# Performance work log

Measured on AMD Instinct MI355X. Metric: run time of the kernel, lower is better.

Reference implementation:

```python
import jax, jax.numpy as jnp
import numpy as np

NUM_HEADS = 8
DIM = 256  # == out_dim; module implicitly requires dim == out_dim


def setup_inputs() -> dict:
    key = jax.random.key(0)
    k0, k1, k2, k3, k4, k5 = jax.random.split(key, 6)
    B, N, T, dim = 4, 128, 128, DIM
    s = dim ** -0.5
    return {
        "v": jax.random.normal(k0, (B, N, T, dim), dtype=jnp.float32),
        "Wq": jax.random.normal(k1, (dim, dim), dtype=jnp.float32) * s,
        "Wk": jax.random.normal(k2, (dim, dim), dtype=jnp.float32) * s,
        "Wv": jax.random.normal(k3, (dim, dim), dtype=jnp.float32) * s,
        "Wp": jax.random.normal(k4, (dim, dim), dtype=jnp.float32) * s,
        "bp": jax.random.normal(k5, (dim,), dtype=jnp.float32) * 0.01,
    }


def reference(v, Wq, Wk, Wv, Wp, bp):
    B, N, T, dim = v.shape
    H = NUM_HEADS
    hd = dim // H
    scale = hd ** -0.5
    # projections (qkv_bias=False)
    q = (v @ Wq).reshape(B * N, T, H, hd)
    k = (v @ Wk).reshape(B * N, T, H, hd)
    vv = (v @ Wv).reshape(B * N, T, H, hd)
    # NOTE: heads axis is NOT moved before the matmul in the original torch
    # code, so attention is over the HEADS axis: per (b*n, t) an HxH matrix.
    attn = jnp.einsum('mthd,mtgd->mthg', q, k) * scale  # [B*N, T, H, H]
    attn = jax.nn.softmax(attn, axis=-1)
    x = jnp.einsum('mthg,mtgd->mthd', attn, vv).reshape(B, N, T, dim)
    # output projection (with bias); dropout probs are 0 / eval mode
    return x @ Wp + bp
```

## Files before the change

### kernel.cpp

```cpp
#include <hip/hip_runtime.h>
#include <hip/hip_bf16.h>
#include <math.h>


#define DIMX      256
#define NH        8
#define HD        32
#define TM        32
#define NTHREADS  256
#define ASTRIDE   264
#define QSTRIDE   776
#define NT_QKV    48
#define NT_P      16
#define KT        8

typedef __bf16 bf16x8 __attribute__((ext_vector_type(8)));
typedef __bf16 bf16x4 __attribute__((ext_vector_type(4)));
typedef float  f32x4  __attribute__((ext_vector_type(4)));

__global__ void pack_weights(const float* __restrict__ Wq,
                             const float* __restrict__ Wk,
                             const float* __restrict__ Wv,
                             const float* __restrict__ Wp,
                             __bf16* __restrict__ pk)
{
    const int QKV_FRAGS = NT_QKV * KT * 64;
    int u = blockIdx.x * blockDim.x + threadIdx.x;
    const float* W;
    int nt, kt, lane;
    if (u < QKV_FRAGS) {
        nt = u / (KT * 64); kt = (u / 64) % KT; lane = u % 64;
        if (nt < 16)      { W = Wq; }
        else if (nt < 32) { W = Wk; nt -= 16; }
        else              { W = Wv; nt -= 32; }
    } else {
        int u2 = u - QKV_FRAGS;
        nt = u2 / (KT * 64); kt = (u2 / 64) % KT; lane = u2 % 64;
        W = Wp;
    }
    const int n  = nt * 16 + (lane & 15);
    const int k0 = kt * 32 + (lane >> 4) * 8;
    bf16x8 frag;
#pragma unroll
    for (int j = 0; j < 8; ++j)
        frag[j] = (__bf16)W[(size_t)(k0 + j) * DIMX + n];
    *(bf16x8*)(pk + (size_t)u * 8) = frag;
}

__global__ __launch_bounds__(NTHREADS, 2)
void fused_attn_mfma(const float* __restrict__ v,
                     const __bf16* __restrict__ Wqkv_pk,
                     const __bf16* __restrict__ Wp_pk,
                     const float* __restrict__ bp,
                     float* __restrict__ out)
{
    __shared__ __align__(16) unsigned short smem[TM * ASTRIDE + TM * QSTRIDE];
    unsigned short* As  = smem;
    unsigned short* QKV = smem + TM * ASTRIDE;

    const int tid   = threadIdx.x;
    const int lane  = tid & 63;
    const int wv_id = tid >> 6;
    const int l15   = lane & 15;
    const int quad  = lane >> 4;
    const long token0 = (long)blockIdx.x * TM;

    {
        const float4* src = (const float4*)(v + token0 * DIMX);
#pragma unroll
        for (int i = 0; i < 8; ++i) {
            int u = tid + NTHREADS * i;
            int m = u >> 6;
            int c = (u & 63) * 4;
            float4 t4 = src[u];
            bf16x4 b4 = { (__bf16)t4.x, (__bf16)t4.y, (__bf16)t4.z, (__bf16)t4.w };
            *(bf16x4*)&As[m * ASTRIDE + c] = b4;
        }
    }
    __syncthreads();

    {
        const int nt0 = wv_id * 12;
        f32x4 acc[2][12];
#pragma unroll
        for (int tt = 0; tt < 2; ++tt)
#pragma unroll
            for (int j = 0; j < 12; ++j)
                acc[tt][j] = (f32x4){0.f, 0.f, 0.f, 0.f};

        for (int kt = 0; kt < KT; ++kt) {
            bf16x8 vf[2];
#pragma unroll
            for (int tt = 0; tt < 2; ++tt)
                vf[tt] = *(const bf16x8*)&As[(tt * 16 + l15) * ASTRIDE + kt * 32 + quad * 8];
            const bf16x8* wb = (const bf16x8*)Wqkv_pk + ((size_t)(nt0 * KT + kt) * 64 + lane);
#pragma unroll
            for (int j = 0; j < 12; ++j) {
                bf16x8 wf = wb[(size_t)j * KT * 64];
                acc[0][j] = __builtin_amdgcn_mfma_f32_16x16x32_bf16(wf, vf[0], acc[0][j], 0, 0, 0);
                acc[1][j] = __builtin_amdgcn_mfma_f32_16x16x32_bf16(wf, vf[1], acc[1][j], 0, 0, 0);
            }
        }
#pragma unroll
        for (int tt = 0; tt < 2; ++tt)
#pragma unroll
            for (int j = 0; j < 12; ++j) {
                bf16x4 p4 = { (__bf16)acc[tt][j][0], (__bf16)acc[tt][j][1],
                              (__bf16)acc[tt][j][2], (__bf16)acc[tt][j][3] };
                *(bf16x4*)&QKV[(tt * 16 + l15) * QSTRIDE + (nt0 + j) * 16 + quad * 4] = p4;
            }
    }
    __syncthreads();

    {
        const int ta = tid >> 3;
        const int h  = tid & 7;
        const float scale = 0.17677669529663687f;
        const unsigned short* qrow = &QKV[ta * QSTRIDE + h * HD];
        const unsigned short* kbase = &QKV[ta * QSTRIDE + 256];
        const unsigned short* vbase = &QKV[ta * QSTRIDE + 512];

        float q[HD];
#pragma unroll
        for (int s = 0; s < 4; ++s) {
            bf16x8 t = *(const bf16x8*)(qrow + s * 8);
#pragma unroll
            for (int j = 0; j < 8; ++j) q[s * 8 + j] = (float)t[j];
        }
        float logits[NH];
#pragma unroll
        for (int g = 0; g < NH; ++g) {
            float s = 0.f;
#pragma unroll
            for (int sg = 0; sg < 4; ++sg) {
                bf16x8 t = *(const bf16x8*)(kbase + g * HD + sg * 8);
#pragma unroll
                for (int j = 0; j < 8; ++j) s += q[sg * 8 + j] * (float)t[j];
            }
            logits[g] = s * scale;
        }
        float mx = logits[0];
#pragma unroll
        for (int g = 1; g < NH; ++g) mx = fmaxf(mx, logits[g]);
        float se = 0.f;
#pragma unroll
        for (int g = 0; g < NH; ++g) { logits[g] = __expf(logits[g] - mx); se += logits[g]; }
        float inv = 1.f / se;
#pragma unroll
        for (int g = 0; g < NH; ++g) logits[g] *= inv;

        float x[HD];
#pragma unroll
        for (int d = 0; d < HD; ++d) x[d] = 0.f;
#pragma unroll
        for (int g = 0; g < NH; ++g) {
            float p = logits[g];
#pragma unroll
            for (int sg = 0; sg < 4; ++sg) {
                bf16x8 t = *(const bf16x8*)(vbase + g * HD + sg * 8);
#pragma unroll
                for (int j = 0; j < 8; ++j) x[sg * 8 + j] += p * (float)t[j];
            }
        }
#pragma unroll
        for (int s = 0; s < 4; ++s) {
            bf16x8 o;
#pragma unroll
            for (int j = 0; j < 8; ++j) o[j] = (__bf16)x[s * 8 + j];
            *(bf16x8*)&As[ta * ASTRIDE + h * HD + s * 8] = o;
        }
    }
    __syncthreads();

    {
        const int nt0 = wv_id * 4;
        f32x4 acc[2][4];
#pragma unroll
        for (int tt = 0; tt < 2; ++tt)
#pragma unroll
            for (int j = 0; j < 4; ++j)
                acc[tt][j] = (f32x4){0.f, 0.f, 0.f, 0.f};

        for (int kt = 0; kt < KT; ++kt) {
            bf16x8 xf[2];
#pragma unroll
            for (int tt = 0; tt < 2; ++tt)
                xf[tt] = *(const bf16x8*)&As[(tt * 16 + l15) * ASTRIDE + kt * 32 + quad * 8];
            const bf16x8* wb = (const bf16x8*)Wp_pk + ((size_t)(nt0 * KT + kt) * 64 + lane);
#pragma unroll
            for (int j = 0; j < 4; ++j) {
                bf16x8 wf = wb[(size_t)j * KT * 64];
                acc[0][j] = __builtin_amdgcn_mfma_f32_16x16x32_bf16(wf, xf[0], acc[0][j], 0, 0, 0);
                acc[1][j] = __builtin_amdgcn_mfma_f32_16x16x32_bf16(wf, xf[1], acc[1][j], 0, 0, 0);
            }
        }
#pragma unroll
        for (int j = 0; j < 4; ++j) {
            f32x4 b = *(const f32x4*)&bp[(nt0 + j) * 16 + quad * 4];
#pragma unroll
            for (int tt = 0; tt < 2; ++tt) {
                f32x4 o = acc[tt][j] + b;
                *(f32x4*)&out[(token0 + tt * 16 + l15) * DIMX + (nt0 + j) * 16 + quad * 4] = o;
            }
        }
    }
}

extern "C" void kernel_launch(void* const* d_in, const int* in_sizes, int n_in,
                              void* d_out, int out_size, void* d_ws, size_t ws_size,
                              hipStream_t stream) {
    const float* v  = (const float*)d_in[0];
    const float* Wq = (const float*)d_in[1];
    const float* Wk = (const float*)d_in[2];
    const float* Wv = (const float*)d_in[3];
    const float* Wp = (const float*)d_in[4];
    const float* bp = (const float*)d_in[5];
    float* out = (float*)d_out;

    __bf16* pk = (__bf16*)d_ws;
    const __bf16* Wqkv_pk = pk;
    const __bf16* Wp_pk   = pk + (size_t)24576 * 8;

    pack_weights<<<128, 256, 0, stream>>>(Wq, Wk, Wv, Wp, pk);

    const int ntokens = in_sizes[0] / DIMX;
    fused_attn_mfma<<<ntokens / TM, NTHREADS, 0, stream>>>(v, Wqkv_pk, Wp_pk, bp, out);
}
```

Before: 188.1 us.

## Double block threads, split head attention across lane pairs, prefetch weight fragments

Raises the block to 512 threads, so each of 8 waves computes half as many MFMA output tiles in both projections. The per-head attention step is split across two lanes, each handling 16 of the 32 head dimensions, and the partial logits are combined with a shuffle. A software prefetch of the next k-step's weight fragments is added to hide global load latency. This lowers per-thread register pressure and lets more waves run concurrently, at the cost of an extra barrier and more redundant activation fragment loads per wave.

```diff
diff --git a/kernel.cpp b/kernel.cpp
--- a/kernel.cpp
+++ b/kernel.cpp
@@ -7,12 +7,13 @@
 #define NH        8
 #define HD        32
 #define TM        32
-#define NTHREADS  256
+#define NTHREADS  512
 #define ASTRIDE   264
 #define QSTRIDE   776
 #define NT_QKV    48
-#define NT_P      16
 #define KT        8
+#define NJ1       6
+#define NJ2       2
 
 typedef __bf16 bf16x8 __attribute__((ext_vector_type(8)));
 typedef __bf16 bf16x4 __attribute__((ext_vector_type(4)));
@@ -47,7 +48,7 @@
     *(bf16x8*)(pk + (size_t)u * 8) = frag;
 }
 
-__global__ __launch_bounds__(NTHREADS, 2)
+__global__ __launch_bounds__(NTHREADS, 4)
 void fused_attn_mfma(const float* __restrict__ v,
                      const __bf16* __restrict__ Wqkv_pk,
                      const __bf16* __restrict__ Wp_pk,
@@ -68,7 +69,7 @@
     {
         const float4* src = (const float4*)(v + token0 * DIMX);
 #pragma unroll
-        for (int i = 0; i < 8; ++i) {
+        for (int i = 0; i < 4; ++i) {
             int u = tid + NTHREADS * i;
             int m = u >> 6;
             int c = (u & 63) * 4;
@@ -80,31 +81,44 @@
     __syncthreads();
 
     {
-        const int nt0 = wv_id * 12;
-        f32x4 acc[2][12];
+        const int nt0 = wv_id * NJ1;
+        f32x4 acc[2][NJ1];
 #pragma unroll
         for (int tt = 0; tt < 2; ++tt)
 #pragma unroll
-            for (int j = 0; j < 12; ++j)
+            for (int j = 0; j < NJ1; ++j)
                 acc[tt][j] = (f32x4){0.f, 0.f, 0.f, 0.f};
 
+        const bf16x8* wb = (const bf16x8*)Wqkv_pk + lane;
+        bf16x8 wcur[NJ1];
+#pragma unroll
+        for (int j = 0; j < NJ1; ++j)
+            wcur[j] = wb[(size_t)((nt0 + j) * KT) * 64];
+
         for (int kt = 0; kt < KT; ++kt) {
+            const int ktn = (kt + 1 < KT) ? kt + 1 : KT - 1;
+            bf16x8 wnxt[NJ1];
+#pragma unroll
+            for (int j = 0; j < NJ1; ++j)
+                wnxt[j] = wb[(size_t)((nt0 + j) * KT + ktn) * 64];
+
             bf16x8 vf[2];
 #pragma unroll
             for (int tt = 0; tt < 2; ++tt)
                 vf[tt] = *(const bf16x8*)&As[(tt * 16 + l15) * ASTRIDE + kt * 32 + quad * 8];
-            const bf16x8* wb = (const bf16x8*)Wqkv_pk + ((size_t)(nt0 * KT + kt) * 64 + lane);
-#pragma unroll
-            for (int j = 0; j < 12; ++j) {
-                bf16x8 wf = wb[(size_t)j * KT * 64];
-                acc[0][j] = __builtin_amdgcn_mfma_f32_16x16x32_bf16(wf, vf[0], acc[0][j], 0, 0, 0);
-                acc[1][j] = __builtin_amdgcn_mfma_f32_16x16x32_bf16(wf, vf[1], acc[1][j], 0, 0, 0);
-            }
+
+#pragma unroll
+            for (int j = 0; j < NJ1; ++j) {
+                acc[0][j] = __builtin_amdgcn_mfma_f32_16x16x32_bf16(wcur[j], vf[0], acc[0][j], 0, 0, 0);
+                acc[1][j] = __builtin_amdgcn_mfma_f32_16x16x32_bf16(wcur[j], vf[1], acc[1][j], 0, 0, 0);
+            }
+#pragma unroll
+            for (int j = 0; j < NJ1; ++j) wcur[j] = wnxt[j];
         }
 #pragma unroll
         for (int tt = 0; tt < 2; ++tt)
 #pragma unroll
-            for (int j = 0; j < 12; ++j) {
+            for (int j = 0; j < NJ1; ++j) {
                 bf16x4 p4 = { (__bf16)acc[tt][j][0], (__bf16)acc[tt][j][1],
                               (__bf16)acc[tt][j][2], (__bf16)acc[tt][j][3] };
                 *(bf16x4*)&QKV[(tt * 16 + l15) * QSTRIDE + (nt0 + j) * 16 + quad * 4] = p4;
@@ -113,16 +127,19 @@
     __syncthreads();
 
     {
-        const int ta = tid >> 3;
-        const int h  = tid & 7;
+        const int ta  = tid >> 4;
+        const int sub = tid & 15;
+        const int h   = sub >> 1;
+        const int d0  = (sub & 1) * 16;
         const float scale = 0.17677669529663687f;
-        const unsigned short* qrow = &QKV[ta * QSTRIDE + h * HD];
-        const unsigned short* kbase = &QKV[ta * QSTRIDE + 256];
-        const unsigned short* vbase = &QKV[ta * QSTRIDE + 512];
-
-        float q[HD];
-#pragma unroll
-        for (int s = 0; s < 4; ++s) {
+
+        const unsigned short* qrow  = &QKV[ta * QSTRIDE + h * HD + d0];
+        const unsigned short* kbase = &QKV[ta * QSTRIDE + 256 + d0];
+        const unsigned short* vbase = &QKV[ta * QSTRIDE + 512 + d0];
+
+        float q[16];
+#pragma unroll
+        for (int s = 0; s < 2; ++s) {
             bf16x8 t = *(const bf16x8*)(qrow + s * 8);
 #pragma unroll
             for (int j = 0; j < 8; ++j) q[s * 8 + j] = (float)t[j];
@@ -132,13 +149,17 @@
         for (int g = 0; g < NH; ++g) {
             float s = 0.f;
 #pragma unroll
-            for (int sg = 0; sg < 4; ++sg) {
+            for (int sg = 0; sg < 2; ++sg) {
                 bf16x8 t = *(const bf16x8*)(kbase + g * HD + sg * 8);
 #pragma unroll
                 for (int j = 0; j < 8; ++j) s += q[sg * 8 + j] * (float)t[j];
             }
-            logits[g] = s * scale;
-        }
+            logits[g] = s;
+        }
+#pragma unroll
+        for (int g = 0; g < NH; ++g)
+            logits[g] = (logits[g] + __shfl_xor(logits[g], 1, 64)) * scale;
+
         float mx = logits[0];
 #pragma unroll
         for (int g = 1; g < NH; ++g) mx = fmaxf(mx, logits[g]);
@@ -149,53 +170,67 @@
 #pragma unroll
         for (int g = 0; g < NH; ++g) logits[g] *= inv;
 
-        float x[HD];
-#pragma unroll
-        for (int d = 0; d < HD; ++d) x[d] = 0.f;
+        float x[16];
+#pragma unroll
+        for (int d = 0; d < 16; ++d) x[d] = 0.f;
 #pragma unroll
         for (int g = 0; g < NH; ++g) {
             float p = logits[g];
 #pragma unroll
-            for (int sg = 0; sg < 4; ++sg) {
+            for (int sg = 0; sg < 2; ++sg) {
                 bf16x8 t = *(const bf16x8*)(vbase + g * HD + sg * 8);
 #pragma unroll
                 for (int j = 0; j < 8; ++j) x[sg * 8 + j] += p * (float)t[j];
             }
         }
-#pragma unroll
-        for (int s = 0; s < 4; ++s) {
+        __syncthreads();
+#pragma unroll
+        for (int s = 0; s < 2; ++s) {
             bf16x8 o;
 #pragma unroll
             for (int j = 0; j < 8; ++j) o[j] = (__bf16)x[s * 8 + j];
-            *(bf16x8*)&As[ta * ASTRIDE + h * HD + s * 8] = o;
+            *(bf16x8*)&As[ta * ASTRIDE + h * HD + d0 + s * 8] = o;
         }
     }
     __syncthreads();
 
     {
-        const int nt0 = wv_id * 4;
-        f32x4 acc[2][4];
+        const int nt0 = wv_id * NJ2;
+        f32x4 acc[2][NJ2];
 #pragma unroll
         for (int tt = 0; tt < 2; ++tt)
 #pragma unroll
-            for (int j = 0; j < 4; ++j)
+            for (int j = 0; j < NJ2; ++j)
                 acc[tt][j] = (f32x4){0.f, 0.f, 0.f, 0.f};
 
+        const bf16x8* wb = (const bf16x8*)Wp_pk + lane;
+        bf16x8 wcur[NJ2];
+#pragma unroll
+        for (int j = 0; j < NJ2; ++j)
+            wcur[j] = wb[(size_t)((nt0 + j) * KT) * 64];
+
         for (int kt = 0; kt < KT; ++kt) {
+            const int ktn = (kt + 1 < KT) ? kt + 1 : KT - 1;
+            bf16x8 wnxt[NJ2];
+#pragma unroll
+            for (int j = 0; j < NJ2; ++j)
+                wnxt[j] = wb[(size_t)((nt0 + j) * KT + ktn) * 64];
+
             bf16x8 xf[2];
 #pragma unroll
             for (int tt = 0; tt < 2; ++tt)
                 xf[tt] = *(const bf16x8*)&As[(tt * 16 + l15) * ASTRIDE + kt * 32 + quad * 8];
-            const bf16x8* wb = (const bf16x8*)Wp_pk + ((size_t)(nt0 * KT + kt) * 64 + lane);
-#pragma unroll
-            for (int j = 0; j < 4; ++j) {
-                bf16x8 wf = wb[(size_t)j * KT * 64];
-                acc[0][j] = __builtin_amdgcn_mfma_f32_16x16x32_bf16(wf, xf[0], acc[0][j], 0, 0, 0);
-                acc[1][j] = __builtin_amdgcn_mfma_f32_16x16x32_bf16(wf, xf[1], acc[1][j], 0, 0, 0);
-            }
-        }
-#pragma unroll
-        for (int j = 0; j < 4; ++j) {
+
+#pragma unroll
+            for (int j = 0; j < NJ2; ++j) {
+                acc[0][j] = __builtin_amdgcn_mfma_f32_16x16x32_bf16(wcur[j], xf[0], acc[0][j], 0, 0, 0);
+                acc[1][j] = __builtin_amdgcn_mfma_f32_16x16x32_bf16(wcur[j], xf[1], acc[1][j], 0, 0, 0);
+            }
+#pragma unroll
+            for (int j = 0; j < NJ2; ++j) wcur[j] = wnxt[j];
+        }
+#pragma unroll
+        for (int j = 0; j < NJ2; ++j) {
             f32x4 b = *(const f32x4*)&bp[(nt0 + j) * 16 + quad * 4];
 #pragma unroll
             for (int tt = 0; tt < 2; ++tt) {
@@ -221,7 +256,7 @@
     const __bf16* Wqkv_pk = pk;
     const __bf16* Wp_pk   = pk + (size_t)24576 * 8;
 
-    pack_weights<<<128, 256, 0, stream>>>(Wq, Wk, Wv, Wp, pk);
+    pack_weights<<<256, 128, 0, stream>>>(Wq, Wk, Wv, Wp, pk);
 
     const int ntokens = in_sizes[0] / DIMX;
     fused_attn_mfma<<<ntokens / TM, NTHREADS, 0, stream>>>(v, Wqkv_pk, Wp_pk, bp, out);
```

Result: faster. 163.9 us (-12.9%).
